# Performance work log

Measured on AMD Instinct MI355X. Metric: run time of the kernel, lower is better.

Reference implementation:

```python
import jax, jax.numpy as jnp
import numpy as np

D_MODEL = 2048
N_HEADS = 16
D_K = D_MODEL // N_HEADS
D_FF = ((int(D_MODEL * 8 / 3) + 63) // 64) * 64  # 5504
B, S = 2, 2048
EPS = 1e-6


def setup_inputs() -> dict:
    key = jax.random.key(0)
    ks = jax.random.split(key, 16)
    sc = 0.02
    x = jax.random.normal(ks[0], (B, S, D_MODEL), dtype=jnp.float32)
    mask = jnp.tril(jnp.ones((S, S), dtype=jnp.int32))[None]  # [1,S,S] causal
    inp = {
        'x': x,
        'mask': mask,
        'wq': jax.random.normal(ks[1], (D_MODEL, D_MODEL), jnp.float32) * sc,
        'bq': jnp.zeros((D_MODEL,), jnp.float32),
        'wk': jax.random.normal(ks[2], (D_MODEL, D_MODEL), jnp.float32) * sc,
        'bk': jnp.zeros((D_MODEL,), jnp.float32),
        'wv': jax.random.normal(ks[3], (D_MODEL, D_MODEL), jnp.float32) * sc,
        'bv': jnp.zeros((D_MODEL,), jnp.float32),
        'wo': jax.random.normal(ks[4], (D_MODEL, D_MODEL), jnp.float32) * sc,
        'bo': jnp.zeros((D_MODEL,), jnp.float32),
        'g1': jnp.ones((D_MODEL,), jnp.float32),  # RMSNorm weights
        'g2': jnp.ones((D_MODEL,), jnp.float32),
        'w1': jax.random.normal(ks[5], (D_MODEL, D_FF), jnp.float32) * sc,
        'w3': jax.random.normal(ks[6], (D_MODEL, D_FF), jnp.float32) * sc,
        'w2': jax.random.normal(ks[7], (D_FF, D_MODEL), jnp.float32) * sc,
    }
    return inp


def _rmsnorm(x, w):
    rms = jnp.sqrt(jnp.mean(x * x, axis=-1, keepdims=True) + EPS)
    return x / rms * w


def _block(x, mask, wq, bq, wk, bk, wv, bv, wo, bo, g1, g2, w1, w2, w3):
    b, s, _ = x.shape
    # --- attention sublayer (pre-LN) ---
    n = _rmsnorm(x, g1)
    q = (n @ wq + bq).reshape(b, s, N_HEADS, D_K).transpose(0, 2, 1, 3)
    k = (n @ wk + bk).reshape(b, s, N_HEADS, D_K).transpose(0, 2, 1, 3)
    v = (n @ wv + bv).reshape(b, s, N_HEADS, D_K).transpose(0, 2, 1, 3)
    scores = jnp.einsum('bhqd,bhkd->bhqk', q, k) / jnp.sqrt(jnp.float32(D_K))
    m = mask[:, None, :, :]  # [1,1,S,S]
    scores = jnp.where(m == 0, jnp.float32(-jnp.inf), scores)
    attn = jax.nn.softmax(scores, axis=-1)
    ao = jnp.einsum('bhqk,bhkd->bhqd', attn, v)
    ao = ao.transpose(0, 2, 1, 3).reshape(b, s, D_MODEL)
    x = x + (ao @ wo + bo)
    # --- SwiGLU FFN sublayer (pre-LN) ---
    n = _rmsnorm(x, g2)
    ffn = (jax.nn.silu(n @ w1) * (n @ w3)) @ w2
    return x + ffn


def reference(x, mask, wq, bq, wk, bk, wv, bv, wo, bo, g1, g2, w1, w2, w3):
    return _block(x, mask, wq, bq, wk, bk, wv, bv, wo, bo, g1, g2, w1, w2, w3)
```

## Files before the change

kernel.cpp:

```cpp
#include <hip/hip_runtime.h>
#include <stdint.h>

typedef unsigned short u16;
typedef __bf16 bf16x8 __attribute__((ext_vector_type(8)));
typedef float f32x4 __attribute__((ext_vector_type(4)));

#define D_MODEL 2048
#define NHEADS 16
#define DK 128
#define DFF 5504
#define DFFP 5632
#define BB 2
#define SS 2048
#define MTOK 4096
#define DQKV 6144

#define AS1 __attribute__((address_space(1)))
#define AS3 __attribute__((address_space(3)))

__device__ __forceinline__ u16 f2bf(float f){
  union { float f; uint32_t u; } v; v.f = f;
  uint32_t r = v.u + 0x7fffu + ((v.u >> 16) & 1u);
  return (u16)(r >> 16);
}
__device__ __forceinline__ float bf2f(u16 u){
  union { uint32_t u; float f; } v; v.u = ((uint32_t)u) << 16;
  return v.f;
}
__device__ __forceinline__ u16 cvt_bf16(float f){
  union { __bf16 h; u16 u; } v; v.h = (__bf16)f; return v.u;
}
__device__ __forceinline__ float fexp2(float x){
#if __has_builtin(__builtin_amdgcn_exp2f)
  return __builtin_amdgcn_exp2f(x);
#else
  return exp2f(x);
#endif
}

__global__ __launch_bounds__(256) void k_transpose_w(const float* __restrict__ W,
                                                     u16* __restrict__ Wt, int K, int Nsrc){
  __shared__ float tile[32][33];
  int n0 = blockIdx.x * 32, k0 = blockIdx.y * 32;
  int tx = threadIdx.x, ty = threadIdx.y;
  #pragma unroll
  for (int r = 0; r < 4; ++r){
    int n = n0 + tx;
    tile[ty + r*8][tx] = (n < Nsrc) ? W[(size_t)(k0 + ty + r*8) * Nsrc + n] : 0.0f;
  }
  __syncthreads();
  #pragma unroll
  for (int r = 0; r < 4; ++r)
    Wt[(size_t)(n0 + ty + r*8) * K + k0 + tx] = f2bf(tile[tx][ty + r*8]);
}

__global__ __launch_bounds__(256) void k_transpose_v(const u16* __restrict__ V,
                                                     u16* __restrict__ Vt, int ld){
  __shared__ u16 tile[32][33];
  int s0 = blockIdx.x * 32;
  int bh = blockIdx.y >> 2, dt = blockIdx.y & 3;
  int b = bh >> 4, h = bh & 15;
  int tx = threadIdx.x, ty = threadIdx.y;
  #pragma unroll
  for (int r = 0; r < 4; ++r)
    tile[ty + r*8][tx] = V[(size_t)(b*SS + s0 + ty + r*8) * ld + h*DK + dt*32 + tx];
  __syncthreads();
  #pragma unroll
  for (int r = 0; r < 4; ++r)
    Vt[(size_t)(bh*DK + dt*32 + ty + r*8) * SS + s0 + tx] = tile[tx][ty + r*8];
}

__global__ __launch_bounds__(256) void k_concat3(const float* __restrict__ a,
                                                 const float* __restrict__ b,
                                                 const float* __restrict__ c,
                                                 float* __restrict__ o){
  int i = blockIdx.x*256 + threadIdx.x;
  if (i >= DQKV) return;
  o[i] = (i < 2048) ? a[i] : (i < 4096 ? b[i-2048] : c[i-4096]);
}

__global__ __launch_bounds__(256) void k_rmsnorm(const float* __restrict__ X,
                                                 const float* __restrict__ g,
                                                 u16* __restrict__ out){
  int row = blockIdx.x, tid = threadIdx.x;
  const float* x = X + (size_t)row * D_MODEL;
  float4 a = ((const float4*)x)[tid*2];
  float4 b = ((const float4*)x)[tid*2+1];
  float ss = a.x*a.x + a.y*a.y + a.z*a.z + a.w*a.w
           + b.x*b.x + b.y*b.y + b.z*b.z + b.w*b.w;
  #pragma unroll
  for (int m = 1; m < 64; m <<= 1) ss += __shfl_xor(ss, m, 64);
  __shared__ float red[4];
  if ((tid & 63) == 0) red[tid >> 6] = ss;
  __syncthreads();
  float tot = red[0] + red[1] + red[2] + red[3];
  float sc = rsqrtf(tot * (1.0f / D_MODEL) + 1e-6f);
  float4 ga = ((const float4*)g)[tid*2];
  float4 gb = ((const float4*)g)[tid*2+1];
  uint32_t w0 = f2bf(a.x*sc*ga.x) | ((uint32_t)f2bf(a.y*sc*ga.y) << 16);
  uint32_t w1 = f2bf(a.z*sc*ga.z) | ((uint32_t)f2bf(a.w*sc*ga.w) << 16);
  uint32_t w2 = f2bf(b.x*sc*gb.x) | ((uint32_t)f2bf(b.y*sc*gb.y) << 16);
  uint32_t w3 = f2bf(b.z*sc*gb.z) | ((uint32_t)f2bf(b.w*sc*gb.w) << 16);
  ((uint4*)(out + (size_t)row * D_MODEL))[tid] = make_uint4(w0, w1, w2, w3);
}

__global__ __launch_bounds__(256) void k_silu_mul(const u16* __restrict__ a,
                                                  const u16* __restrict__ b,
                                                  u16* __restrict__ o, int n8){
  int i = blockIdx.x * 256 + threadIdx.x;
  if (i >= n8) return;
  uint4 av = ((const uint4*)a)[i];
  uint4 bv = ((const uint4*)b)[i];
  uint32_t aa[4] = {av.x, av.y, av.z, av.w};
  uint32_t bb[4] = {bv.x, bv.y, bv.z, bv.w};
  uint32_t rr[4];
  #pragma unroll
  for (int j = 0; j < 4; ++j){
    float x0 = bf2f((u16)(aa[j] & 0xffff)), x1 = bf2f((u16)(aa[j] >> 16));
    float y0 = bf2f((u16)(bb[j] & 0xffff)), y1 = bf2f((u16)(bb[j] >> 16));
    float r0 = x0 / (1.f + __expf(-x0)) * y0;
    float r1 = x1 / (1.f + __expf(-x1)) * y1;
    rr[j] = f2bf(r0) | ((uint32_t)f2bf(r1) << 16);
  }
  ((uint4*)o)[i] = make_uint4(rr[0], rr[1], rr[2], rr[3]);
}

template<int EPI>
__global__ __launch_bounds__(512, 2) void k_gemm8p(
    const u16* __restrict__ A, const u16* __restrict__ Bt,
    const float* __restrict__ bias, const u16* __restrict__ aux,
    void* __restrict__ Cout, int M, int N, int K,
    int lda, int ldb, int ldc)
{
  extern __shared__ __align__(16) char smem[];
  const int tid = threadIdx.x;
  const int lane = tid & 63, wid = tid >> 6;
  const int wr = wid >> 2, wc = wid & 3;
  const int lrow = lane & 15, lhi = lane >> 4;

  int nwg = gridDim.x, wg = blockIdx.x;
  int nbx = N >> 8, nbm = M >> 8;
  int xcd = wg & 7, sub = wg >> 3;
  int m0, n0;
  if ((nwg & 7) == 0 && (nbm & 1) == 0 && (nbx & 3) == 0){
    int mh = nbm >> 1;
    int mr = sub % mh, nc = sub / mh;
    m0 = (((xcd & 1) * mh) + mr) << 8;
    n0 = (((xcd >> 1) * (nbx >> 2)) + nc) << 8;
  } else {
    int qq = nwg >> 3, rr2 = nwg & 7;
    int swz = (xcd < rr2 ? xcd*(qq+1) : rr2*(qq+1) + (xcd-rr2)*qq) + sub;
    m0 = (swz / nbx) << 8; n0 = (swz % nbx) << 8;
  }

  const int nk = K >> 6;
  const int hA = wr, hB = wc >> 1;
  const int gA = wc;
  const int gB = (wr << 1) | (wc & 1);

  auto stA = [&](int d, int kk, int q){
    #pragma unroll
    for (int L = 0; L < 2; ++L){
      int p = q*8192 + gA*2048 + L*1024 + lane*16;
      int row = p >> 7;
      int o = (p & 127) ^ ((row & 7) << 4);
      __builtin_amdgcn_global_load_lds(
        (const AS1 void*)(A + (size_t)(m0 + hA*128 + row)*lda + kk + (o >> 1)),
        (AS3 void*)(smem + d*65536 + hA*16384 + p), 16, 0, 0);
    }
  };
  auto stB = [&](int d, int kk, int s){
    #pragma unroll
    for (int L = 0; L < 2; ++L){
      int p = s*4096 + (gB >> 1)*8192 + (gB & 1)*2048 + L*1024 + lane*16;
      int row = p >> 7;
      int o = (p & 127) ^ ((row & 7) << 4);
      __builtin_amdgcn_global_load_lds(
        (const AS1 void*)(Bt + (size_t)(n0 + hB*128 + row)*ldb + kk + (o >> 1)),
        (AS3 void*)(smem + d*65536 + 32768 + hB*16384 + p), 16, 0, 0);
    }
  };
  auto rdA = [&](int d, int rloc, int ks)->bf16x8{
    int p = rloc*128 + ((ks*64 + lhi*16) ^ ((rloc & 7) << 4));
    return *(const bf16x8*)(smem + d*65536 + hA*16384 + p);
  };
  auto rdB = [&](int d, int rloc, int ks)->bf16x8{
    int p = rloc*128 + ((ks*64 + lhi*16) ^ ((rloc & 7) << 4));
    return *(const bf16x8*)(smem + d*65536 + 32768 + hB*16384 + p);
  };

  f32x4 acc[8][4] = {};

  stA(0, 0, 0); stB(0, 0, 0); stB(0, 0, 1); stA(0, 0, 1);
  asm volatile("s_waitcnt vmcnt(0)" ::: "memory");
  __builtin_amdgcn_s_barrier();

  for (int t = 0; t < nk; ++t){
    int d = t & 1, dn = d ^ 1, kkn = (t + 1) << 6;
    bool pf = (t + 1 < nk);
    bf16x8 aR[8], bQ0[4], bQ1[4];

    #pragma unroll
    for (int ii = 0; ii < 4; ++ii){
      aR[ii*2]   = rdA(d, ii*16 + lrow, 0);
      aR[ii*2+1] = rdA(d, ii*16 + lrow, 1);
    }
    #pragma unroll
    for (int j = 0; j < 2; ++j){
      bQ0[j*2]   = rdB(d, (wc&1)*64 + j*16 + lrow, 0);
      bQ0[j*2+1] = rdB(d, (wc&1)*64 + j*16 + lrow, 1);
    }
    if (pf){ stA(dn, kkn, 0); stB(dn, kkn, 0); }
    __builtin_amdgcn_s_barrier();
    asm volatile("s_waitcnt lgkmcnt(0)" ::: "memory");
    __builtin_amdgcn_sched_barrier(0);
    __builtin_amdgcn_s_setprio(1);
    #pragma unroll
    for (int ii = 0; ii < 4; ++ii)
      #pragma unroll
      for (int j = 0; j < 2; ++j){
        acc[ii][j] = __builtin_amdgcn_mfma_f32_16x16x32_bf16(aR[ii*2],   bQ0[j*2],   acc[ii][j], 0, 0, 0);
        acc[ii][j] = __builtin_amdgcn_mfma_f32_16x16x32_bf16(aR[ii*2+1], bQ0[j*2+1], acc[ii][j], 0, 0, 0);
      }
    __builtin_amdgcn_s_setprio(0);
    if (pf) asm volatile("s_waitcnt vmcnt(6)" ::: "memory");
    else    asm volatile("s_waitcnt vmcnt(2)" ::: "memory");
    __builtin_amdgcn_sched_barrier(0);
    __builtin_amdgcn_s_barrier();

    #pragma unroll
    for (int j = 0; j < 2; ++j){
      bQ1[j*2]   = rdB(d, (wc&1)*64 + 32 + j*16 + lrow, 0);
      bQ1[j*2+1] = rdB(d, (wc&1)*64 + 32 + j*16 + lrow, 1);
    }
    if (pf) stB(dn, kkn, 1);
    __builtin_amdgcn_s_barrier();
    asm volatile("s_waitcnt lgkmcnt(0)" ::: "memory");
    __builtin_amdgcn_sched_barrier(0);
    __builtin_amdgcn_s_setprio(1);
    #pragma unroll
    for (int ii = 0; ii < 4; ++ii)
      #pragma unroll
      for (int j = 0; j < 2; ++j){
        acc[ii][2+j] = __builtin_amdgcn_mfma_f32_16x16x32_bf16(aR[ii*2],   bQ1[j*2],   acc[ii][2+j], 0, 0, 0);
        acc[ii][2+j] = __builtin_amdgcn_mfma_f32_16x16x32_bf16(aR[ii*2+1], bQ1[j*2+1], acc[ii][2+j], 0, 0, 0);
      }
    __builtin_amdgcn_s_setprio(0);
    if (pf) asm volatile("s_waitcnt vmcnt(6)" ::: "memory");
    else    asm volatile("s_waitcnt vmcnt(0)" ::: "memory");
    __builtin_amdgcn_sched_barrier(0);
    __builtin_amdgcn_s_barrier();

    #pragma unroll
    for (int ii = 0; ii < 4; ++ii){
      aR[ii*2]   = rdA(d, 64 + ii*16 + lrow, 0);
      aR[ii*2+1] = rdA(d, 64 + ii*16 + lrow, 1);
    }
    if (pf) stA(dn, kkn, 1);
    __builtin_amdgcn_s_barrier();
    asm volatile("s_waitcnt lgkmcnt(0)" ::: "memory");
    __builtin_amdgcn_sched_barrier(0);
    __builtin_amdgcn_s_setprio(1);
    #pragma unroll
    for (int ii = 0; ii < 4; ++ii)
      #pragma unroll
      for (int j = 0; j < 2; ++j){
        acc[4+ii][2+j] = __builtin_amdgcn_mfma_f32_16x16x32_bf16(aR[ii*2],   bQ1[j*2],   acc[4+ii][2+j], 0, 0, 0);
        acc[4+ii][2+j] = __builtin_amdgcn_mfma_f32_16x16x32_bf16(aR[ii*2+1], bQ1[j*2+1], acc[4+ii][2+j], 0, 0, 0);
      }
    __builtin_amdgcn_s_setprio(0);
    __builtin_amdgcn_s_barrier();

    __builtin_amdgcn_s_setprio(1);
    #pragma unroll
    for (int ii = 0; ii < 4; ++ii)
      #pragma unroll
      for (int j = 0; j < 2; ++j){
        acc[4+ii][j] = __builtin_amdgcn_mfma_f32_16x16x32_bf16(aR[ii*2],   bQ0[j*2],   acc[4+ii][j], 0, 0, 0);
        acc[4+ii][j] = __builtin_amdgcn_mfma_f32_16x16x32_bf16(aR[ii*2+1], bQ0[j*2+1], acc[4+ii][j], 0, 0, 0);
      }
    __builtin_amdgcn_s_setprio(0);
    if (pf) asm volatile("s_waitcnt vmcnt(4)" ::: "memory");
    __builtin_amdgcn_sched_barrier(0);
    __builtin_amdgcn_s_barrier();
  }

  u16* Cw = (u16*)Cout;
  int cofs = 0;
  if constexpr (EPI == 5){
    if (n0 >= 5632){ Cw = (u16*)aux; cofs = 5632; }
  }
  #pragma unroll
  for (int i = 0; i < 8; ++i){
    #pragma unroll
    for (int j = 0; j < 4; ++j){
      int col = n0 + wc*64 + j*16 + lrow;
      float bv = 0.f;
      if constexpr (EPI == 0) bv = bias[col];
      #pragma unroll
      for (int q = 0; q < 4; ++q){
        int row = m0 + wr*128 + i*16 + lhi*4 + q;
        float v = acc[i][j][q] + bv;
        Cw[(size_t)row*ldc + (col - cofs)] = f2bf(v);
      }
    }
  }
}

template<int EPI>
__global__ __launch_bounds__(256) void k_gemm_bt(
    const u16* __restrict__ A, const u16* __restrict__ Bt,
    const float* __restrict__ bias, const float* __restrict__ res,
    const u16* __restrict__ aux,
    void* __restrict__ Cout, int M, int N, int K,
    int lda, int ldb, int ldc)
{
  __shared__ __align__(16) u16 As[3][128*32];
  __shared__ __align__(16) u16 Bs[3][128*32];
  int tid = threadIdx.x;

  int nwg = gridDim.x, wg = blockIdx.x;
  int qq = nwg >> 3, rr = nwg & 7;
  int xcd = wg & 7, sub = wg >> 3;
  int swz = (xcd < rr ? xcd*(qq+1) : rr*(qq+1) + (xcd-rr)*qq) + sub;
  int nbx = N >> 7;
  int m0 = (swz / nbx) << 7, n0 = (swz % nbx) << 7;

  int lane = tid & 63, wave = tid >> 6;
  int wr = wave >> 1, wc = wave & 1;
  int lrow = lane & 15, lhi = lane >> 4;
  f32x4 acc[4][4] = {};
  int srow = tid >> 2;
  int schk = tid & 3;
  const int nk = K >> 5;

  auto stage = [&](int slot, int kt){
    int k0 = kt << 5;
    int c = schk ^ (srow & 3);
    #pragma unroll
    for (int cc = 0; cc < 2; ++cc){
      int r = cc*64 + srow;
      __builtin_amdgcn_global_load_lds(
        (const AS1 void*)(A + (size_t)(m0 + r)*lda + k0 + c*8),
        (AS3 void*)(&As[slot][r*32 + schk*8]), 16, 0, 0);
      __builtin_amdgcn_global_load_lds(
        (const AS1 void*)(Bt + (size_t)(n0 + r)*ldb + k0 + c*8),
        (AS3 void*)(&Bs[slot][r*32 + schk*8]), 16, 0, 0);
    }
  };

  stage(0, 0);
  if (nk > 1) stage(1, 1);
  if (nk > 1) asm volatile("s_waitcnt vmcnt(4)" ::: "memory");
  else        asm volatile("s_waitcnt vmcnt(0)" ::: "memory");
  __builtin_amdgcn_s_barrier();

  for (int kt = 0; kt < nk; ++kt){
    int cur = kt % 3;
    if (kt + 2 < nk) stage((kt + 2) % 3, kt + 2);
    int rchk = lhi ^ (lrow & 3);
    bf16x8 af[4], bfv[4];
    #pragma unroll
    for (int i = 0; i < 4; ++i){
      af[i]  = *(const bf16x8*)(&As[cur][(wr*64 + i*16 + lrow)*32 + rchk*8]);
      bfv[i] = *(const bf16x8*)(&Bs[cur][(wc*64 + i*16 + lrow)*32 + rchk*8]);
    }
    #pragma unroll
    for (int i = 0; i < 4; ++i)
      #pragma unroll
      for (int j = 0; j < 4; ++j)
        acc[i][j] = __builtin_amdgcn_mfma_f32_16x16x32_bf16(af[i], bfv[j], acc[i][j], 0, 0, 0);
    if (kt + 2 < nk) asm volatile("s_waitcnt vmcnt(4)" ::: "memory");
    else             asm volatile("s_waitcnt vmcnt(0)" ::: "memory");
    __builtin_amdgcn_s_barrier();
  }

  #pragma unroll
  for (int i = 0; i < 4; ++i){
    #pragma unroll
    for (int j = 0; j < 4; ++j){
      int col = n0 + wc*64 + j*16 + lrow;
      float bv = 0.f;
      if constexpr (EPI == 0 || EPI == 1) bv = bias[col];
      #pragma unroll
      for (int q = 0; q < 4; ++q){
        int row = m0 + wr*64 + i*16 + lhi*4 + q;
        size_t idx = (size_t)row*ldc + col;
        float v = acc[i][j][q] + bv;
        if constexpr (EPI == 1 || EPI == 3) v += res[idx];
        if constexpr (EPI == 4){
          float a0 = bf2f(aux[idx]);
          v = a0 / (1.f + __expf(-a0)) * v;
        }
        if constexpr (EPI == 0 || EPI == 2 || EPI == 4) ((u16*)Cout)[idx] = f2bf(v);
        else ((float*)Cout)[idx] = v;
      }
    }
  }
}

__global__ __launch_bounds__(512) void k_attn(
    const u16* __restrict__ Q, const u16* __restrict__ Kb,
    const u16* __restrict__ Vt, u16* __restrict__ O, int ldq)
{
  int tid = threadIdx.x, lane = tid & 63, wave = tid >> 6;
  int lrow = lane & 15, lhi = lane >> 4;
  int bidx = blockIdx.x;
  int bh = bidx >> 3, j = bidx & 7;
  int b = bh >> 4, h = bh & 15;

  __shared__ __align__(16) u16 Kbuf[2][64*128];
  __shared__ __align__(16) u16 Vbuf[2][128*64];
  __shared__ __align__(16) u16 P_lds[8][16*64];
  char* pw = (char*)&P_lds[wave][0];
  const float sc2 = 0.08838834764831845f * 1.44269504088896340736f;

  auto stage = [&](int bufi, int kt){
    int kv0 = kt << 6;
    char* kd = (char*)&Kbuf[bufi][0];
    char* vd = (char*)&Vbuf[bufi][0];
    #pragma unroll
    for (int L = 0; L < 2; ++L){
      int cid = wave*128 + L*64 + lane;
      int r = cid >> 4, c = cid & 15;
      int cg = c ^ (r & 7);
      __builtin_amdgcn_global_load_lds(
        (const AS1 void*)(Kb + (size_t)(b*SS + kv0 + r)*ldq + h*DK + cg*8),
        (AS3 void*)(kd + wave*2048 + L*1024 + lane*16), 16, 0, 0);
      int dd = cid >> 3, c8 = cid & 7;
      int cv = c8 ^ (dd & 7);
      __builtin_amdgcn_global_load_lds(
        (const AS1 void*)(Vt + (size_t)bh*DK*SS + (size_t)dd*SS + kv0 + cv*8),
        (AS3 void*)(vd + wave*2048 + L*1024 + lane*16), 16, 0, 0);
    }
  };

  #pragma unroll 1
  for (int item = 0; item < 2; ++item){
    int qi = item == 0 ? 15 - j : j;
    int qs = qi * 128;
    int nt = 2*qi + 2;
    int qrow = qs + wave * 16;

    bf16x8 qf[4];
    const u16* qbase = Q + (size_t)(b*SS + qrow + lrow)*ldq + h*DK + lhi*8;
    #pragma unroll
    for (int dc = 0; dc < 4; ++dc) qf[dc] = *(const bf16x8*)(qbase + dc*32);

    f32x4 accO[8] = {};
    float mr[4] = {-1e30f,-1e30f,-1e30f,-1e30f};
    float lr[4] = {0.f,0.f,0.f,0.f};

    stage(0, 0);
    __syncthreads();

    for (int kt = 0; kt < nt; ++kt){
      int cur = kt & 1;
      if (kt + 1 < nt) stage(cur ^ 1, kt + 1);
      int kv0 = kt << 6;
      if (kv0 <= qrow + 15){
        const char* kl = (const char*)&Kbuf[cur][0];
        const char* vl = (const char*)&Vbuf[cur][0];
        bool domask = (kv0 + 63 > qrow);

        f32x4 sf[4];
        #pragma unroll
        for (int hf = 0; hf < 4; ++hf){
          int rl = hf*16 + lrow;
          int sw = rl & 7;
          f32x4 a = {};
          #pragma unroll
          for (int dc = 0; dc < 4; ++dc){
            bf16x8 kf = *(const bf16x8*)(kl + rl*256 + (((lhi + dc*4) ^ sw) << 4));
            a = __builtin_amdgcn_mfma_f32_16x16x32_bf16(qf[dc], kf, a, 0, 0, 0);
          }
          sf[hf] = a;
        }

        float p[4][4], mx[4];
        #pragma unroll
        for (int q = 0; q < 4; ++q){
          float s0 = sf[0][q]*sc2, s1 = sf[1][q]*sc2, s2 = sf[2][q]*sc2, s3 = sf[3][q]*sc2;
          if (domask){
            int qg = qrow + lhi*4 + q;
            if (kv0      + lrow > qg) s0 = -1e30f;
            if (kv0 + 16 + lrow > qg) s1 = -1e30f;
            if (kv0 + 32 + lrow > qg) s2 = -1e30f;
            if (kv0 + 48 + lrow > qg) s3 = -1e30f;
          }
          p[q][0]=s0; p[q][1]=s1; p[q][2]=s2; p[q][3]=s3;
          float m = fmaxf(fmaxf(s0,s1), fmaxf(s2,s3));
          m = fmaxf(m, __shfl_xor(m, 1, 64));
          m = fmaxf(m, __shfl_xor(m, 2, 64));
          m = fmaxf(m, __shfl_xor(m, 4, 64));
          m = fmaxf(m, __shfl_xor(m, 8, 64));
          mx[q] = m;
        }
        float dmax = fmaxf(fmaxf(mx[0]-mr[0], mx[1]-mr[1]), fmaxf(mx[2]-mr[2], mx[3]-mr[3]));
        bool rescale = !__all(dmax <= 8.0f);
        float al[4];
        #pragma unroll
        for (int q = 0; q < 4; ++q){
          if (rescale){
            float mn = fmaxf(mr[q], mx[q]);
            al[q] = fexp2(mr[q] - mn);
            mr[q] = mn;
          } else al[q] = 1.0f;
          p[q][0] = fexp2(p[q][0] - mr[q]);
          p[q][1] = fexp2(p[q][1] - mr[q]);
          p[q][2] = fexp2(p[q][2] - mr[q]);
          p[q][3] = fexp2(p[q][3] - mr[q]);
          float sm = (p[q][0] + p[q][1]) + (p[q][2] + p[q][3]);
          sm += __shfl_xor(sm, 1, 64);
          sm += __shfl_xor(sm, 2, 64);
          sm += __shfl_xor(sm, 4, 64);
          sm += __shfl_xor(sm, 8, 64);
          lr[q] = lr[q]*al[q] + sm;
        }
        if (rescale){
          #pragma unroll
          for (int f = 0; f < 8; ++f)
            #pragma unroll
            for (int q = 0; q < 4; ++q) accO[f][q] *= al[q];
        }

        #pragma unroll
        for (int q = 0; q < 4; ++q){
          int row = lhi*4 + q;
          int rb = row*128, sw = (row & 7) << 4;
          #pragma unroll
          for (int hf = 0; hf < 4; ++hf)
            *(u16*)(pw + rb + ((hf*32 + lrow*2) ^ sw)) = cvt_bf16(p[q][hf]);
        }
        __builtin_amdgcn_sched_barrier(0);
        int rsw = (lrow & 7) << 4;
        bf16x8 pa0 = *(const bf16x8*)(pw + lrow*128 + ((     lhi*16) ^ rsw));
        bf16x8 pa1 = *(const bf16x8*)(pw + lrow*128 + ((64 + lhi*16) ^ rsw));

        #pragma unroll
        for (int f = 0; f < 8; ++f){
          int d = f*16 + lrow;
          int swv = d & 7;
          bf16x8 v0 = *(const bf16x8*)(vl + d*128 + (((lhi    ) ^ swv) << 4));
          bf16x8 v1 = *(const bf16x8*)(vl + d*128 + (((lhi + 4) ^ swv) << 4));
          accO[f] = __builtin_amdgcn_mfma_f32_16x16x32_bf16(pa0, v0, accO[f], 0, 0, 0);
          accO[f] = __builtin_amdgcn_mfma_f32_16x16x32_bf16(pa1, v1, accO[f], 0, 0, 0);
        }
      }
      __syncthreads();
    }

    #pragma unroll
    for (int q = 0; q < 4; ++q){
      float inv = 1.0f / lr[q];
      #pragma unroll
      for (int f = 0; f < 8; ++f){
        int row = b*SS + qrow + lhi*4 + q;
        int col = h*DK + f*16 + lrow;
        O[(size_t)row*D_MODEL + col] = cvt_bf16(accO[f][q] * inv);
      }
    }
    __syncthreads();
  }
}

extern "C" void kernel_launch(void* const* d_in, const int* in_sizes, int n_in,
                              void* d_out, int out_size, void* d_ws, size_t ws_size,
                              hipStream_t stream)
{
  (void)in_sizes; (void)n_in; (void)out_size;
  const float* x  = (const float*)d_in[0];
  const float* wq = (const float*)d_in[2];
  const float* bq = (const float*)d_in[3];
  const float* wk = (const float*)d_in[4];
  const float* bk = (const float*)d_in[5];
  const float* wv = (const float*)d_in[6];
  const float* bv = (const float*)d_in[7];
  const float* wo = (const float*)d_in[8];
  const float* bo = (const float*)d_in[9];
  const float* g1 = (const float*)d_in[10];
  const float* g2 = (const float*)d_in[11];
  const float* w1 = (const float*)d_in[12];
  const float* w3 = (const float*)d_in[13];
  const float* w2 = (const float*)d_in[14];
  float* out = (float*)d_out;

  const size_t MB = 1u << 20;
  const size_t W2T_B = (size_t)D_MODEL * DFF * sizeof(u16);
  const size_t NEED = 152*MB + W2T_B + 32768;
  if (ws_size < NEED) return;
  char* ws = (char*)d_ws;
  u16* bufA  = (u16*)(ws + 0);
  u16* qkv   = (u16*)(ws + 16*MB);
  u16* h1    = qkv;
  u16* wqkvt = (u16*)(ws + 64*MB);
  u16* w1w3t = (u16*)(ws + 64*MB);
  u16* wot   = (u16*)(ws + 88*MB);
  u16* vtb   = (u16*)(ws + 96*MB);
  u16* h3    = (u16*)(ws + 108*MB);
  u16* w2t   = (u16*)(ws + 152*MB);
  float* bqkv = (float*)(ws + 152*MB + W2T_B);

  bool big = true;
  big &= hipFuncSetAttribute((const void*)k_gemm8p<0>, hipFuncAttributeMaxDynamicSharedMemorySize, 131072) == hipSuccess;
  big &= hipFuncSetAttribute((const void*)k_gemm8p<5>, hipFuncAttributeMaxDynamicSharedMemorySize, 131072) == hipSuccess;

  dim3 tb(32, 8);
  k_transpose_w<<<dim3(64,64), tb, 0, stream>>>(wq, wqkvt,               D_MODEL, D_MODEL);
  k_transpose_w<<<dim3(64,64), tb, 0, stream>>>(wk, wqkvt + 2048*2048,   D_MODEL, D_MODEL);
  k_transpose_w<<<dim3(64,64), tb, 0, stream>>>(wv, wqkvt + 2*2048*2048, D_MODEL, D_MODEL);
  k_transpose_w<<<dim3(64,64), tb, 0, stream>>>(wo, wot, D_MODEL, D_MODEL);
  k_transpose_w<<<dim3(64, DFF/32), tb, 0, stream>>>(w2, w2t, DFF, D_MODEL);
  k_concat3<<<24, 256, 0, stream>>>(bq, bk, bv, bqkv);

  k_rmsnorm<<<MTOK, 256, 0, stream>>>(x, g1, bufA);
  if (big)
    k_gemm8p<0><<<(MTOK/256)*(DQKV/256), 512, 131072, stream>>>(bufA, wqkvt, bqkv, nullptr, qkv, MTOK, DQKV, D_MODEL, D_MODEL, D_MODEL, DQKV);
  else
    k_gemm_bt<0><<<(DQKV/128)*(MTOK/128), 256, 0, stream>>>(bufA, wqkvt, bqkv, nullptr, nullptr, qkv, MTOK, DQKV, D_MODEL, D_MODEL, D_MODEL, DQKV);
  k_transpose_v<<<dim3(SS/32, 128), tb, 0, stream>>>(qkv + 4096, vtb, DQKV);
  k_transpose_w<<<dim3(DFFP/32, 64), tb, 0, stream>>>(w1, w1w3t, D_MODEL, DFF);
  k_attn<<<dim3(BB*NHEADS*8), 512, 0, stream>>>(qkv, qkv + 2048, vtb, bufA, DQKV);
  k_gemm_bt<1><<<16*32, 256, 0, stream>>>(bufA, wot, bo, x, nullptr, out, MTOK, D_MODEL, D_MODEL, D_MODEL, D_MODEL, D_MODEL);
  k_transpose_w<<<dim3(DFFP/32, 64), tb, 0, stream>>>(w3, w1w3t + (size_t)DFFP*2048, D_MODEL, DFF);
  k_rmsnorm<<<MTOK, 256, 0, stream>>>(out, g2, bufA);
  if (big){
    k_gemm8p<5><<<(MTOK/256)*((2*DFFP)/256), 512, 131072, stream>>>(bufA, w1w3t, nullptr, h3, h1, MTOK, 2*DFFP, D_MODEL, D_MODEL, D_MODEL, DFFP);
  } else {
    k_gemm_bt<2><<<(DFFP/128)*32, 256, 0, stream>>>(bufA, w1w3t, nullptr, nullptr, nullptr, h1, MTOK, DFFP, D_MODEL, D_MODEL, D_MODEL, DFFP);
    k_gemm_bt<2><<<(DFFP/128)*32, 256, 0, stream>>>(bufA, w1w3t + (size_t)DFFP*2048, nullptr, nullptr, nullptr, h3, MTOK, DFFP, D_MODEL, D_MODEL, D_MODEL, DFFP);
  }
  k_silu_mul<<<(MTOK*DFFP/8 + 255)/256, 256, 0, stream>>>(h1, h3, h1, MTOK*DFFP/8);
  k_gemm_bt<3><<<16*32, 256, 0, stream>>>(h1, w2t, nullptr, out, nullptr, out, MTOK, D_MODEL, DFF, DFFP, DFF, D_MODEL);
}
```

Before: 721.8 us.

## Split-K the down-projection GEMM onto the large-tile kernel with fp32 partials

Adds an EPI==6 mode to the 256x256 GEMM kernel. The grid is split into two halves, each computing half of the K dimension (DFF/2) of the w2 down-projection and writing fp32 partials to workspace buffers. A new elementwise kernel then adds both partials into the residual output. The goal is to move the w2 GEMM from the smaller-tile kernel to the faster large-tile MFMA kernel while keeping enough workgroups to fill the device. The cost is extra fp32 partial writes and reads, plus one more kernel launch.

```diff
diff --git a/kernel.cpp b/kernel.cpp
--- a/kernel.cpp
+++ b/kernel.cpp
@@ -125,6 +125,19 @@
   ((uint4*)o)[i] = make_uint4(rr[0], rr[1], rr[2], rr[3]);
 }
 
+__global__ __launch_bounds__(256) void k_add2(float* __restrict__ out,
+                                              const float* __restrict__ p0,
+                                              const float* __restrict__ p1, int n4){
+  int stride = gridDim.x * 256;
+  for (int i = blockIdx.x * 256 + threadIdx.x; i < n4; i += stride){
+    float4 o = ((const float4*)out)[i];
+    float4 a = ((const float4*)p0)[i];
+    float4 b = ((const float4*)p1)[i];
+    o.x += a.x + b.x; o.y += a.y + b.y; o.z += a.z + b.z; o.w += a.w + b.w;
+    ((float4*)out)[i] = o;
+  }
+}
+
 template<int EPI>
 __global__ __launch_bounds__(512, 2) void k_gemm8p(
     const u16* __restrict__ A, const u16* __restrict__ Bt,
@@ -139,6 +152,15 @@
   const int lrow = lane & 15, lhi = lane >> 4;
 
   int nwg = gridDim.x, wg = blockIdx.x;
+  int ksl = 0;
+  if constexpr (EPI == 6){
+    int hn = nwg >> 1;
+    if (wg >= hn){ ksl = 1; wg -= hn; }
+    nwg = hn;
+    A  += (size_t)ksl * K;
+    Bt += (size_t)ksl * K;
+  }
+
   int nbx = N >> 8, nbm = M >> 8;
   int xcd = wg & 7, sub = wg >> 3;
   int m0, n0;
@@ -285,6 +307,21 @@
     __builtin_amdgcn_s_barrier();
   }
 
+  if constexpr (EPI == 6){
+    float* P = ksl ? (float*)aux : (float*)Cout;
+    #pragma unroll
+    for (int i = 0; i < 8; ++i)
+      #pragma unroll
+      for (int j = 0; j < 4; ++j){
+        int col = n0 + wc*64 + j*16 + lrow;
+        #pragma unroll
+        for (int q = 0; q < 4; ++q){
+          int row = m0 + wr*128 + i*16 + lhi*4 + q;
+          P[(size_t)row*ldc + col] = acc[i][j][q];
+        }
+      }
+    return;
+  }
   u16* Cw = (u16*)Cout;
   int cofs = 0;
   if constexpr (EPI == 5){
@@ -598,12 +635,15 @@
   u16* wot   = (u16*)(ws + 88*MB);
   u16* vtb   = (u16*)(ws + 96*MB);
   u16* h3    = (u16*)(ws + 108*MB);
+  float* p0  = (float*)(ws + 64*MB);
+  float* p1  = (float*)(ws + 96*MB);
   u16* w2t   = (u16*)(ws + 152*MB);
   float* bqkv = (float*)(ws + 152*MB + W2T_B);
 
   bool big = true;
   big &= hipFuncSetAttribute((const void*)k_gemm8p<0>, hipFuncAttributeMaxDynamicSharedMemorySize, 131072) == hipSuccess;
   big &= hipFuncSetAttribute((const void*)k_gemm8p<5>, hipFuncAttributeMaxDynamicSharedMemorySize, 131072) == hipSuccess;
+  big &= hipFuncSetAttribute((const void*)k_gemm8p<6>, hipFuncAttributeMaxDynamicSharedMemorySize, 131072) == hipSuccess;
 
   dim3 tb(32, 8);
   k_transpose_w<<<dim3(64,64), tb, 0, stream>>>(wq, wqkvt,               D_MODEL, D_MODEL);
@@ -626,10 +666,13 @@
   k_rmsnorm<<<MTOK, 256, 0, stream>>>(out, g2, bufA);
   if (big){
     k_gemm8p<5><<<(MTOK/256)*((2*DFFP)/256), 512, 131072, stream>>>(bufA, w1w3t, nullptr, h3, h1, MTOK, 2*DFFP, D_MODEL, D_MODEL, D_MODEL, DFFP);
+    k_silu_mul<<<(MTOK*DFFP/8 + 255)/256, 256, 0, stream>>>(h1, h3, h1, MTOK*DFFP/8);
+    k_gemm8p<6><<<2*(MTOK/256)*(D_MODEL/256), 512, 131072, stream>>>(h1, w2t, nullptr, (const u16*)p1, p0, MTOK, D_MODEL, DFF/2, DFFP, DFF, D_MODEL);
+    k_add2<<<2048, 256, 0, stream>>>(out, p0, p1, MTOK*D_MODEL/4);
   } else {
     k_gemm_bt<2><<<(DFFP/128)*32, 256, 0, stream>>>(bufA, w1w3t, nullptr, nullptr, nullptr, h1, MTOK, DFFP, D_MODEL, D_MODEL, D_MODEL, DFFP);
     k_gemm_bt<2><<<(DFFP/128)*32, 256, 0, stream>>>(bufA, w1w3t + (size_t)DFFP*2048, nullptr, nullptr, nullptr, h3, MTOK, DFFP, D_MODEL, D_MODEL, D_MODEL, DFFP);
-  }
-  k_silu_mul<<<(MTOK*DFFP/8 + 255)/256, 256, 0, stream>>>(h1, h3, h1, MTOK*DFFP/8);
-  k_gemm_bt<3><<<16*32, 256, 0, stream>>>(h1, w2t, nullptr, out, nullptr, out, MTOK, D_MODEL, DFF, DFFP, DFF, D_MODEL);
-}
+    k_silu_mul<<<(MTOK*DFFP/8 + 255)/256, 256, 0, stream>>>(h1, h3, h1, MTOK*DFFP/8);
+    k_gemm_bt<3><<<16*32, 256, 0, stream>>>(h1, w2t, nullptr, out, nullptr, out, MTOK, D_MODEL, DFF, DFFP, DFF, D_MODEL);
+  }
+}
```

Measured after the change: 671.7 us. 6.9% less time.
